# Kernel optimization log

Measured on AMD Instinct MI355X. Metric: run time of the kernel, lower is better.

The kernel has to match this reference:

```python
import jax, jax.numpy as jnp
import numpy as np

SIZE = 84        # pupil size
SIZE_F = 167     # field grid size
X_PAD = 39       # pad for 90 -> 167
KNUM = 16        # number of phase kernels (== required batch size)
CENTER = 120     # center crop
NOISE = 0.003


def _disk_mask(M=SIZE, R=SIZE / 2.0):
    # get_amp: unit disk of radius R on an MxM grid
    x, y = np.meshgrid(np.arange(-(M - 1) / 2, M / 2), np.arange(-(M - 1) / 2, M / 2))
    return jnp.asarray((x ** 2 + y ** 2 <= R ** 2).astype(np.float32))


def setup_inputs() -> dict:
    key = jax.random.key(0)
    k1, k2, k3 = jax.random.split(key, 3)
    x = jax.random.uniform(k1, (16, 90, 90, 1), dtype=jnp.float32)
    P = jax.random.uniform(k2, (16, 84, 84), dtype=jnp.float32,
                           minval=-0.5 * np.pi, maxval=0.5 * np.pi)
    W3 = jax.random.normal(k3, (12800, 10), dtype=jnp.float32) * 0.01
    b3 = jnp.zeros((10,), dtype=jnp.float32)
    return {"x": x, "P": P, "W3": W3, "b3": b3}


def _forward(x, P, W3, b3):
    mask = _disk_mask()
    amp = jnp.sum(mask)  # normalization of the autocorrelation

    # --- input field: pad 90 -> 167, complex, fftshift/fft2/fftshift ---
    # NOTE: tf.signal.fftshift default shifts ALL axes (incl. batch); the two
    # shifts cancel on the batch axis, replicated faithfully here.
    xp = jnp.pad(x, ((0, 0), (X_PAD, X_PAD - 1), (X_PAD, X_PAD - 1), (0, 0)))[..., 0]
    xc = xp.astype(jnp.complex64)
    X = jnp.fft.fftshift(jnp.fft.fft2(jnp.fft.fftshift(xc)))  # [16,167,167]
    Xr = jnp.repeat(X, KNUM, axis=0)                          # [256,167,167]

    # --- OTF: FFT-accelerated autocorrelation of the pupil P_amp*exp(i*phase) ---
    Pc = (mask * jnp.cos(P) + 1j * mask * jnp.sin(P)).astype(jnp.complex64)  # [16,84,84]
    Pp = jnp.pad(Pc, ((0, 0), (42, 41), (42, 41)))                           # [16,167,167]
    F = jnp.fft.fft2(Pp)
    OTF = jnp.fft.fftshift(jnp.fft.ifft2(F * jnp.conj(F)))  # all-axes shift
    OTF = jnp.concatenate([OTF[8:], OTF[:8]], axis=0) / amp  # undoes batch roll

    # --- propagation: multiply in frequency domain, back to space ---
    y = Xr * jnp.tile(OTF, (KNUM, 1, 1))  # [256,167,167]
    y = jnp.fft.fftshift(jnp.fft.ifft2(jnp.fft.fftshift(y)))
    r = jnp.real(y).reshape(16, KNUM, SIZE_F, SIZE_F)
    # per image: kernels 0..7 minus kernels 8..15 -> channels
    d = jnp.transpose(r[:, :8] - r[:, 8:], (0, 2, 3, 1))  # [16,167,167,8]

    # additive noise (np.random in original; fixed key -> deterministic constant)
    d = d + NOISE * jax.random.normal(jax.random.key(42), d.shape, dtype=jnp.float32)

    # center crop, relu, 3x3/3 max-pool, flatten, softmax dense
    b = (SIZE_F + 1) // 2 - CENTER // 2  # 24
    c = jax.nn.relu(d[:, b:b + CENTER, b:b + CENTER, :])  # [16,120,120,8]
    pooled = jax.lax.reduce_window(c, -jnp.inf, jax.lax.max,
                                   (1, 3, 3, 1), (1, 3, 3, 1), 'VALID')  # [16,40,40,8]
    flat = pooled.reshape(16, -1)  # [16,12800]
    return jax.nn.softmax(flat @ W3 + b3)


def reference(x, P, W3, b3):
    return _forward(x, P, W3, b3)
```

## Files before the change

### kernel.cpp

```cpp
#include <hip/hip_runtime.h>
#include <math.h>

constexpr int N  = 167;
constexpr int NN = 167 * 167;
constexpr int NP = 90;
constexpr int MP = 84;
constexpr int CROP = 120;
constexpr int HCOL = 84;
constexpr int HALF_SZ = 1784896;

constexpr size_t SZ_MAT   = (size_t)NN * 2;
constexpr size_t OFF_M1   = 0;
constexpr size_t OFF_M1T  = OFF_M1 + SZ_MAT;
constexpr size_t OFF_WF   = OFF_M1T + SZ_MAT;
constexpr size_t OFF_M2   = OFF_WF + SZ_MAT;
constexpr size_t OFF_M2T  = OFF_M2 + SZ_MAT;
constexpr size_t OFF_M3   = OFF_M2T + SZ_MAT;
constexpr size_t OFF_M3T84= OFF_M3 + (size_t)CROP * N * 2;
constexpr size_t OFF_PHI2 = OFF_M3T84 + (size_t)HCOL * CROP * 2;
constexpr size_t OFF_AMP  = OFF_PHI2 + (size_t)N * 2;
constexpr size_t OFF_X    = OFF_AMP + 2;
constexpr size_t OFF_T1   = OFF_X  + (size_t)16 * N * HCOL * 2;
constexpr size_t OFF_A    = OFF_T1 + (size_t)16 * N * NP * 2;
constexpr size_t OFF_T2   = OFF_A  + (size_t)16 * NN * 2;
constexpr size_t OFF_BD   = OFF_T2 + (size_t)16 * N * MP * 2;
constexpr size_t OFF_T3   = OFF_BD + (size_t)8 * NN;
constexpr size_t OFF_OTF  = OFF_T3 + (size_t)8 * N * HCOL * 2;
constexpr size_t OFF_FLAT = OFF_OTF+ (size_t)8 * N * HCOL * 2;
constexpr size_t OFF_PC   = OFF_FLAT + (size_t)16 * 12800;
constexpr size_t WS_FLOATS = OFF_PC + (size_t)16 * MP * MP * 2;

__device__ __forceinline__ unsigned rotl32(unsigned x, int r) {
    return (x << r) | (x >> (32 - r));
}

__device__ float noise_at(unsigned idx) {
    unsigned c0, c1; int lane;
    if (idx < (unsigned)HALF_SZ) { c0 = idx; c1 = idx + HALF_SZ; lane = 0; }
    else                         { c0 = idx - HALF_SZ; c1 = idx; lane = 1; }
    const unsigned ks0 = 0u, ks1 = 42u, ks2 = 0x1BD11BDAu ^ 42u;
    unsigned x0 = c0 + ks0, x1 = c1 + ks1;
#define TFR(r) { x0 += x1; x1 = rotl32(x1, r); x1 ^= x0; }
    TFR(13) TFR(15) TFR(26) TFR(6)   x0 += ks1; x1 += ks2 + 1u;
    TFR(17) TFR(29) TFR(16) TFR(24)  x0 += ks2; x1 += ks0 + 2u;
    TFR(13) TFR(15) TFR(26) TFR(6)   x0 += ks0; x1 += ks1 + 3u;
    TFR(17) TFR(29) TFR(16) TFR(24)  x0 += ks1; x1 += ks2 + 4u;
    TFR(13) TFR(15) TFR(26) TFR(6)   x0 += ks2; x1 += ks0 + 5u;
#undef TFR
    unsigned bits = lane ? x1 : x0;
    float u01 = __uint_as_float((bits >> 9) | 0x3F800000u) - 1.0f;
    const float lo = -0.99999994f;
    float f = fmaxf(lo, u01 * 2.0f + lo);
    float w = -log1pf(-f * f);
    float p;
    if (w < 5.0f) {
        w -= 2.5f;
        p = 2.81022636e-08f;
        p = fmaf(p, w, 3.43273939e-07f);
        p = fmaf(p, w, -3.5233877e-06f);
        p = fmaf(p, w, -4.39150654e-06f);
        p = fmaf(p, w, 0.00021858087f);
        p = fmaf(p, w, -0.00125372503f);
        p = fmaf(p, w, -0.00417768164f);
        p = fmaf(p, w, 0.246640727f);
        p = fmaf(p, w, 1.50140941f);
    } else {
        w = sqrtf(w) - 3.0f;
        p = -0.000200214257f;
        p = fmaf(p, w, 0.000100950558f);
        p = fmaf(p, w, 0.00134934322f);
        p = fmaf(p, w, -0.00367342844f);
        p = fmaf(p, w, 0.00573950773f);
        p = fmaf(p, w, -0.0076224613f);
        p = fmaf(p, w, 0.00943887047f);
        p = fmaf(p, w, 1.00167406f);
        p = fmaf(p, w, 2.83297682f);
    }
    return 1.41421356237f * p * f;
}

__global__ void k_prep(const float* __restrict__ P, float* ws) {
    int bx = blockIdx.x, t = threadIdx.x;
    if (bx < 109) {
        int id = bx * 256 + t;
        if (id >= NN) return;
        int k = id / N, m = id % N;
        const float TPI = (float)(6.283185307179586476925286766559 / 167.0);
        float s1, c1, sw, cw, s2, c2;
        int t1 = (int)(((long long)(k + 84) * ((m + 83) % N)) % N);
        sincosf(TPI * (float)t1, &s1, &c1);
        ws[OFF_M1 + 2 * id] = c1;  ws[OFF_M1 + 2 * id + 1] = -s1;
        ws[OFF_M1T + 2 * (m * N + k)] = c1;  ws[OFF_M1T + 2 * (m * N + k) + 1] = -s1;
        int tw = (int)(((long long)k * m) % N);
        sincosf(TPI * (float)tw, &sw, &cw);
        ws[OFF_WF + 2 * id] = cw;  ws[OFF_WF + 2 * id + 1] = -sw;
        int t2 = (int)(((long long)(k + 84) * m) % N);
        sincosf(TPI * (float)t2, &s2, &c2);
        const float inv = 1.0f / 167.0f;
        ws[OFF_M2 + 2 * id] = c2 * inv;  ws[OFF_M2 + 2 * id + 1] = s2 * inv;
        ws[OFF_M2T + 2 * (m * N + k)] = c2 * inv;  ws[OFF_M2T + 2 * (m * N + k) + 1] = s2 * inv;
        if (k < CROP) {
            int t3 = (int)(((long long)(k + 108) * ((m + 83) % N)) % N);
            float s3, c3;
            sincosf(TPI * (float)t3, &s3, &c3);
            ws[OFF_M3 + 2 * (k * N + m)] = c3 * inv;  ws[OFF_M3 + 2 * (k * N + m) + 1] = s3 * inv;
            if (m < HCOL) {
                ws[OFF_M3T84 + 2 * (m * CROP + k)] = c3 * inv;
                ws[OFF_M3T84 + 2 * (m * CROP + k) + 1] = s3 * inv;
            }
        }
        if (id < N) {
            int tp = (2 * id) % N;
            float sp, cp;
            sincosf(TPI * (float)tp, &sp, &cp);
            ws[OFF_PHI2 + 2 * id] = cp;
            ws[OFF_PHI2 + 2 * id + 1] = sp;
        }
    } else if (bx < 550) {
        int id = (bx - 109) * 256 + t;
        if (id >= 16 * MP * MP) return;
        int rc = id % (MP * MP);
        int r = rc / MP, c = rc % MP;
        float y = r - 41.5f, x = c - 41.5f;
        float2 v = {0.f, 0.f};
        if (x * x + y * y <= 1764.0f) {
            float sp, cp; sincosf(P[id], &sp, &cp);
            v.x = cp; v.y = sp;
        }
        ((float2*)(ws + OFF_PC))[id] = v;
    } else {
        __shared__ int red[256];
        int cnt = 0;
        for (int i = t; i < MP * MP; i += 256) {
            int r = i / MP, c = i % MP;
            float y = r - 41.5f, x = c - 41.5f;
            if (x * x + y * y <= 1764.0f) cnt++;
        }
        red[t] = cnt; __syncthreads();
        for (int s = 128; s > 0; s >>= 1) { if (t < s) red[t] += red[t + s]; __syncthreads(); }
        if (t == 0) ws[OFF_AMP] = (float)red[0];
    }
}

__global__ __launch_bounds__(128) void k_rows(const float* __restrict__ x, float* ws) {
    int kr = blockIdx.x, bj = blockIdx.y, t = threadIdx.x;
    __shared__ float2 wbuf[NP];
    if (blockIdx.z == 0) {
        const float2* M1 = (const float2*)(ws + OFF_M1);
        if (t < NP) wbuf[t] = M1[kr * N + 39 + t];
        __syncthreads();
        if (t >= NP) return;
        float2 acc = {0.f, 0.f};
        for (int nr = 0; nr < NP; nr++) {
            float2 w = wbuf[nr];
            float xv = x[(bj * NP + nr) * NP + t];
            acc.x += w.x * xv; acc.y += w.y * xv;
        }
        ((float2*)(ws + OFF_T1))[(bj * N + kr) * NP + t] = acc;
    } else {
        const float2* WF = (const float2*)(ws + OFF_WF);
        if (t < MP) wbuf[t] = WF[kr * N + 42 + t];
        __syncthreads();
        if (t >= MP) return;
        const float2* PC = (const float2*)(ws + OFF_PC) + (size_t)bj * MP * MP;
        float2 acc = {0.f, 0.f};
        for (int nr = 0; nr < MP; nr++) {
            float2 w = wbuf[nr];
            float2 pc = PC[nr * MP + t];
            acc.x += w.x * pc.x - w.y * pc.y;
            acc.y += w.x * pc.y + w.y * pc.x;
        }
        ((float2*)(ws + OFF_T2))[(bj * N + kr) * MP + t] = acc;
    }
}

constexpr int RCH = 6;
__global__ __launch_bounds__(192) void k_cols(float* ws) {
    int bj = blockIdx.y, tid = threadIdx.x;
    __shared__ float2 sbuf[RCH * MP];
    if (blockIdx.x < 84) {
        int k0 = blockIdx.x * 2;
        const float2* T1 = (const float2*)(ws + OFF_T1);
        for (int idx = tid; idx < 2 * NP; idx += 192) {
            int r = idx / NP, m = idx % NP;
            if (k0 + r < N) sbuf[r * NP + m] = T1[((size_t)bj * N + k0 + r) * NP + m];
        }
        __syncthreads();
        int col = tid % HCOL, grp = tid / HCOL;
        if (grp >= 2) return;
        int kr = k0 + grp;
        if (kr >= N) return;
        const float2* M1T = (const float2*)(ws + OFF_M1T);
        float2 acc = {0.f, 0.f};
        for (int nc = 0; nc < NP; nc++) {
            float2 u = sbuf[grp * NP + nc];
            float2 w = M1T[(39 + nc) * N + col];
            acc.x += u.x * w.x - u.y * w.y;
            acc.y += u.x * w.y + u.y * w.x;
        }
        ((float2*)(ws + OFF_X))[((size_t)bj * N + kr) * HCOL + col] = acc;
    } else {
        int i0 = (blockIdx.x - 84) * RCH;
        const float2* T2 = (const float2*)(ws + OFF_T2);
        for (int idx = tid; idx < RCH * MP; idx += 192) {
            int q = idx / MP, nc = idx % MP, kr = i0 + q;
            if (kr < N) sbuf[idx] = T2[(bj * N + kr) * MP + nc];
        }
        __syncthreads();
        if (tid >= N) return;
        const float2* WF = (const float2*)(ws + OFF_WF);
        float2 acc[RCH];
#pragma unroll
        for (int q = 0; q < RCH; q++) acc[q] = make_float2(0.f, 0.f);
        for (int nc = 0; nc < MP; nc++) {
            float2 w = WF[(42 + nc) * N + tid];
#pragma unroll
            for (int q = 0; q < RCH; q++) {
                float2 u = sbuf[q * MP + nc];
                acc[q].x += u.x * w.x - u.y * w.y;
                acc[q].y += u.x * w.y + u.y * w.x;
            }
        }
        float2* A = (float2*)(ws + OFF_A);
#pragma unroll
        for (int q = 0; q < RCH; q++)
            if (i0 + q < N) A[((size_t)bj * N + i0 + q) * N + tid] = acc[q];
    }
}

__global__ __launch_bounds__(192) void k2c(float* ws) {
    int chunk = blockIdx.x, c = blockIdx.y, tid = threadIdx.x;
    int k0 = chunk * 2;
    __shared__ float bds[2][N];
    const float2* A = (const float2*)(ws + OFF_A);
    float inv_amp = 1.0f / ws[OFF_AMP];
    for (int idx = tid; idx < 2 * N; idx += 192) {
        int r = idx / N, m = idx % N;
        int k = k0 + r;
        if (k < N) {
            float2 a0 = A[((size_t)c * N + k) * N + m];
            float2 a1 = A[((size_t)(c + 8) * N + k) * N + m];
            bds[r][m] = (a0.x * a0.x + a0.y * a0.y - a1.x * a1.x - a1.y * a1.y) * inv_amp;
        }
    }
    __syncthreads();
    int col = tid % HCOL, grp = tid / HCOL;
    if (grp >= 2) return;
    int k = k0 + grp;
    if (k >= N) return;
    const float2* M2T = (const float2*)(ws + OFF_M2T);
    float2 acc = {0.f, 0.f};
    for (int m = 0; m < N; m++) {
        float bv = bds[grp][m];
        float2 w = M2T[m * N + col];
        acc.x += w.x * bv; acc.y += w.y * bv;
    }
    ((float2*)(ws + OFF_T3))[((size_t)c * N + k) * HCOL + col] = acc;
}

__global__ __launch_bounds__(192) void k2d(float* ws) {
    int chunk = blockIdx.x, c = blockIdx.y, tid = threadIdx.x;
    int i0 = chunk * 2;
    __shared__ float2 m2s[2][N];
    const float2* M2 = (const float2*)(ws + OFF_M2);
    for (int idx = tid; idx < 2 * N; idx += 192) {
        int r = idx / N, k = idx % N;
        if (i0 + r < N) m2s[r][k] = M2[(i0 + r) * N + k];
    }
    __syncthreads();
    int col = tid % HCOL, grp = tid / HCOL;
    if (grp >= 2) return;
    int i = i0 + grp;
    if (i >= N) return;
    const float2* T3 = (const float2*)(ws + OFF_T3) + (size_t)c * N * HCOL;
    float2 acc = {0.f, 0.f};
    for (int k = 0; k < N; k++) {
        float2 w = m2s[grp][k];
        float2 u = T3[k * HCOL + col];
        acc.x += u.x * w.x - u.y * w.y;
        acc.y += u.x * w.y + u.y * w.x;
    }
    ((float2*)(ws + OFF_OTF))[((size_t)c * N + i) * HCOL + col] = acc;
}

constexpr int K34R = 12;
constexpr int KCH  = 16;
__global__ __launch_bounds__(256) void k34(float* ws) {
    int chunk = blockIdx.x, c = blockIdx.y, b = blockIdx.z, tid = threadIdx.x;
    int i0 = chunk * K34R;
    __shared__ __align__(16) float2 zs[KCH][HCOL];
    __shared__ float2 m3c[K34R][KCH];
    __shared__ __align__(16) float2 us[K34R][HCOL];
    __shared__ float2 phis[N];
    __shared__ float pm[4][CROP];
    const float2* M3  = (const float2*)(ws + OFF_M3);
    const float2* X   = (const float2*)(ws + OFF_X)   + (size_t)b * N * HCOL;
    const float2* OTF = (const float2*)(ws + OFF_OTF) + (size_t)c * N * HCOL;
    for (int idx = tid; idx < N; idx += 256) phis[idx] = ((const float2*)(ws + OFF_PHI2))[idx];

    int p = tid % 42, grp = tid / 42;
    int r0 = grp * 2, r1 = r0 + 1;
    float2 a00 = {0.f,0.f}, a01 = {0.f,0.f}, a10 = {0.f,0.f}, a11 = {0.f,0.f};

    for (int kr0 = 0; kr0 < N; kr0 += KCH) {
        int chn = min(KCH, N - kr0);
        __syncthreads();
        for (int idx = tid; idx < chn * HCOL; idx += 256) {
            int kl = idx / HCOL, col = idx % HCOL;
            float2 xv = X[(kr0 + kl) * HCOL + col];
            float2 ov = OTF[(kr0 + kl) * HCOL + col];
            zs[kl][col] = make_float2(xv.x * ov.x - xv.y * ov.y,
                                      xv.x * ov.y + xv.y * ov.x);
        }
        for (int idx = tid; idx < K34R * KCH; idx += 256) {
            int r = idx / KCH, kl = idx % KCH;
            if (kl < chn) m3c[r][kl] = M3[(i0 + r) * N + kr0 + kl];
        }
        __syncthreads();
        if (grp < 6) {
#pragma unroll 4
            for (int kl = 0; kl < chn; kl++) {
                float4 zz = *(const float4*)&zs[kl][2 * p];
                float2 w0 = m3c[r0][kl], w1 = m3c[r1][kl];
                a00.x += w0.x * zz.x - w0.y * zz.y;  a00.y += w0.x * zz.y + w0.y * zz.x;
                a01.x += w0.x * zz.z - w0.y * zz.w;  a01.y += w0.x * zz.w + w0.y * zz.z;
                a10.x += w1.x * zz.x - w1.y * zz.y;  a10.y += w1.x * zz.y + w1.y * zz.x;
                a11.x += w1.x * zz.z - w1.y * zz.w;  a11.y += w1.x * zz.w + w1.y * zz.z;
            }
        }
    }
    __syncthreads();
    if (grp < 6) {
        us[r0][2 * p] = a00;  us[r0][2 * p + 1] = a01;
        us[r1][2 * p] = a10;  us[r1][2 * p + 1] = a11;
    }
    __syncthreads();
    if (tid < 240) {
        int grp2 = tid / CROP, j = tid % CROP;
        int rbase = grp2 * 6;
        const float2* M3T84 = (const float2*)(ws + OFF_M3T84);
        float2 A[6]; float Bq[6];
#pragma unroll
        for (int q = 0; q < 6; q++) A[q] = make_float2(0.f, 0.f);
        for (int nc = 0; nc < HCOL - 1; nc++) {
            float2 w = M3T84[nc * CROP + j];
#pragma unroll
            for (int q = 0; q < 6; q++) {
                float2 u = us[rbase + q][nc];
                A[q].x += u.x * w.x - u.y * w.y;
                A[q].y += u.x * w.y + u.y * w.x;
            }
        }
        {
            float2 w = M3T84[(HCOL - 1) * CROP + j];
#pragma unroll
            for (int q = 0; q < 6; q++) {
                float2 u = us[rbase + q][HCOL - 1];
                Bq[q] = u.x * w.x - u.y * w.y;
            }
        }
#pragma unroll
        for (int g = 0; g < 2; g++) {
            float vmax = 0.f;
#pragma unroll
            for (int r = 0; r < 3; r++) {
                int q = g * 3 + r, i = i0 + rbase + q;
                int s = i + j + 49; if (s >= N) s -= N;
                float2 ph = phis[s];
                float val = A[q].x * (1.0f + ph.x) - A[q].y * ph.y + Bq[q];
                unsigned idx = (((unsigned)b * N + (24 + i)) * N + (24 + j)) * 8u + c;
                val += 0.003f * noise_at(idx);
                vmax = fmaxf(vmax, val);
            }
            pm[grp2 * 2 + g][j] = vmax;
        }
    }
    __syncthreads();
    if (tid < 160) {
        int pr = tid / 40, pc = tid % 40;
        float m = fmaxf(fmaxf(pm[pr][3 * pc], pm[pr][3 * pc + 1]), pm[pr][3 * pc + 2]);
        int prow = chunk * 4 + pr;
        ws[OFF_FLAT + (size_t)b * 12800 + ((size_t)prow * 40 + pc) * 8 + c] = m;
    }
}

__global__ void k5(const float* __restrict__ W3, const float* __restrict__ b3,
                   const float* __restrict__ ws, float* __restrict__ out) {
    int b = blockIdx.x, t = threadIdx.x;
    __shared__ float red[256][10];
    float acc[10];
#pragma unroll
    for (int o = 0; o < 10; o++) acc[o] = 0.f;
    const float* fl = ws + OFF_FLAT + (size_t)b * 12800;
    for (int f = t; f < 12800; f += 256) {
        float v = fl[f];
#pragma unroll
        for (int o = 0; o < 10; o++) acc[o] = fmaf(v, W3[f * 10 + o], acc[o]);
    }
#pragma unroll
    for (int o = 0; o < 10; o++) red[t][o] = acc[o];
    __syncthreads();
    for (int s = 128; s > 0; s >>= 1) {
        if (t < s) {
#pragma unroll
            for (int o = 0; o < 10; o++) red[t][o] += red[t + s][o];
        }
        __syncthreads();
    }
    if (t == 0) {
        float lg[10], mx = -1e30f;
#pragma unroll
        for (int o = 0; o < 10; o++) { lg[o] = red[0][o] + b3[o]; mx = fmaxf(mx, lg[o]); }
        float sum = 0.f;
#pragma unroll
        for (int o = 0; o < 10; o++) { lg[o] = expf(lg[o] - mx); sum += lg[o]; }
#pragma unroll
        for (int o = 0; o < 10; o++) out[b * 10 + o] = lg[o] / sum;
    }
}

extern "C" void kernel_launch(void* const* d_in, const int* in_sizes, int n_in,
                              void* d_out, int out_size, void* d_ws, size_t ws_size,
                              hipStream_t stream) {
    const float* x  = (const float*)d_in[0];
    const float* P  = (const float*)d_in[1];
    const float* W3 = (const float*)d_in[2];
    const float* b3 = (const float*)d_in[3];
    float* ws  = (float*)d_ws;
    float* out = (float*)d_out;

    k_prep<<<551, 256, 0, stream>>>(P, ws);
    k_rows<<<dim3(N, 16, 2), 128, 0, stream>>>(x, ws);
    k_cols<<<dim3(84 + 28, 16), 192, 0, stream>>>(ws);
    k2c<<<dim3(84, 8), 192, 0, stream>>>(ws);
    k2d<<<dim3(84, 8), 192, 0, stream>>>(ws);
    k34<<<dim3(CROP / K34R, 8, 16), 256, 0, stream>>>(ws);
    k5<<<16, 256, 0, stream>>>(W3, b3, ws, out);
}
```

Measured before the change: 210.7 us.

## Double-buffer k34 tiles, widen row block to 24, use twiddle table in prep

The main k34 kernel now processes 24 output rows per block instead of 12, with each thread computing a 4x2 register tile. The shared-memory tiles are double-buffered, so the next tile's global loads are issued into registers before computing on the current tile. This halves the number of blocks, which halves the redundant X*OTF product and phase reloads per row, and it hides load latency at the cost of more registers and shared memory. The prep kernel also replaces four sincosf calls per element with lookups into a 167-entry shared twiddle table.

```diff
diff --git a/kernel.cpp b/kernel.cpp
--- a/kernel.cpp
+++ b/kernel.cpp
@@ -82,39 +82,41 @@
 __global__ void k_prep(const float* __restrict__ P, float* ws) {
     int bx = blockIdx.x, t = threadIdx.x;
     if (bx < 109) {
+        __shared__ float2 wtab[N];
+        const float TPI = (float)(6.283185307179586476925286766559 / 167.0);
+        for (int i = t; i < N; i += 256) {
+            float s, c; sincosf(TPI * (float)i, &s, &c);
+            wtab[i] = make_float2(c, s);
+        }
+        __syncthreads();
         int id = bx * 256 + t;
         if (id >= NN) return;
         int k = id / N, m = id % N;
-        const float TPI = (float)(6.283185307179586476925286766559 / 167.0);
-        float s1, c1, sw, cw, s2, c2;
-        int t1 = (int)(((long long)(k + 84) * ((m + 83) % N)) % N);
-        sincosf(TPI * (float)t1, &s1, &c1);
-        ws[OFF_M1 + 2 * id] = c1;  ws[OFF_M1 + 2 * id + 1] = -s1;
-        ws[OFF_M1T + 2 * (m * N + k)] = c1;  ws[OFF_M1T + 2 * (m * N + k) + 1] = -s1;
-        int tw = (int)(((long long)k * m) % N);
-        sincosf(TPI * (float)tw, &sw, &cw);
-        ws[OFF_WF + 2 * id] = cw;  ws[OFF_WF + 2 * id + 1] = -sw;
-        int t2 = (int)(((long long)(k + 84) * m) % N);
-        sincosf(TPI * (float)t2, &s2, &c2);
         const float inv = 1.0f / 167.0f;
-        ws[OFF_M2 + 2 * id] = c2 * inv;  ws[OFF_M2 + 2 * id + 1] = s2 * inv;
-        ws[OFF_M2T + 2 * (m * N + k)] = c2 * inv;  ws[OFF_M2T + 2 * (m * N + k) + 1] = s2 * inv;
+        int t1 = ((k + 84) * ((m + 83) % N)) % N;
+        float2 w1 = wtab[t1];
+        ws[OFF_M1 + 2 * id] = w1.x;  ws[OFF_M1 + 2 * id + 1] = -w1.y;
+        ws[OFF_M1T + 2 * (m * N + k)] = w1.x;  ws[OFF_M1T + 2 * (m * N + k) + 1] = -w1.y;
+        int tw = (k * m) % N;
+        float2 ww = wtab[tw];
+        ws[OFF_WF + 2 * id] = ww.x;  ws[OFF_WF + 2 * id + 1] = -ww.y;
+        int t2 = ((k + 84) * m) % N;
+        float2 w2 = wtab[t2];
+        ws[OFF_M2 + 2 * id] = w2.x * inv;  ws[OFF_M2 + 2 * id + 1] = w2.y * inv;
+        ws[OFF_M2T + 2 * (m * N + k)] = w2.x * inv;  ws[OFF_M2T + 2 * (m * N + k) + 1] = w2.y * inv;
         if (k < CROP) {
-            int t3 = (int)(((long long)(k + 108) * ((m + 83) % N)) % N);
-            float s3, c3;
-            sincosf(TPI * (float)t3, &s3, &c3);
-            ws[OFF_M3 + 2 * (k * N + m)] = c3 * inv;  ws[OFF_M3 + 2 * (k * N + m) + 1] = s3 * inv;
+            int t3 = ((k + 108) * ((m + 83) % N)) % N;
+            float2 w3 = wtab[t3];
+            ws[OFF_M3 + 2 * (k * N + m)] = w3.x * inv;  ws[OFF_M3 + 2 * (k * N + m) + 1] = w3.y * inv;
             if (m < HCOL) {
-                ws[OFF_M3T84 + 2 * (m * CROP + k)] = c3 * inv;
-                ws[OFF_M3T84 + 2 * (m * CROP + k) + 1] = s3 * inv;
+                ws[OFF_M3T84 + 2 * (m * CROP + k)] = w3.x * inv;
+                ws[OFF_M3T84 + 2 * (m * CROP + k) + 1] = w3.y * inv;
             }
         }
         if (id < N) {
-            int tp = (2 * id) % N;
-            float sp, cp;
-            sincosf(TPI * (float)tp, &sp, &cp);
-            ws[OFF_PHI2 + 2 * id] = cp;
-            ws[OFF_PHI2 + 2 * id + 1] = sp;
+            float2 wp = wtab[(2 * id) % N];
+            ws[OFF_PHI2 + 2 * id] = wp.x;
+            ws[OFF_PHI2 + 2 * id + 1] = wp.y;
         }
     } else if (bx < 550) {
         int id = (bx - 109) * 256 + t;
@@ -283,69 +285,132 @@
     ((float2*)(ws + OFF_OTF))[((size_t)c * N + i) * HCOL + col] = acc;
 }
 
-constexpr int K34R = 12;
+constexpr int K34R = 24;
 constexpr int KCH  = 16;
+constexpr int NT34 = (N + KCH - 1) / KCH;
 __global__ __launch_bounds__(256) void k34(float* ws) {
     int chunk = blockIdx.x, c = blockIdx.y, b = blockIdx.z, tid = threadIdx.x;
     int i0 = chunk * K34R;
-    __shared__ __align__(16) float2 zs[KCH][HCOL];
-    __shared__ float2 m3c[K34R][KCH];
+    __shared__ __align__(16) float2 zs[2][KCH][HCOL];
+    __shared__ __align__(16) float2 m3c[2][KCH][K34R];
     __shared__ __align__(16) float2 us[K34R][HCOL];
     __shared__ float2 phis[N];
-    __shared__ float pm[4][CROP];
+    __shared__ float pm[8][CROP];
     const float2* M3  = (const float2*)(ws + OFF_M3);
     const float2* X   = (const float2*)(ws + OFF_X)   + (size_t)b * N * HCOL;
     const float2* OTF = (const float2*)(ws + OFF_OTF) + (size_t)c * N * HCOL;
     for (int idx = tid; idx < N; idx += 256) phis[idx] = ((const float2*)(ws + OFF_PHI2))[idx];
 
-    int p = tid % 42, grp = tid / 42;
-    int r0 = grp * 2, r1 = r0 + 1;
-    float2 a00 = {0.f,0.f}, a01 = {0.f,0.f}, a10 = {0.f,0.f}, a11 = {0.f,0.f};
-
-    for (int kr0 = 0; kr0 < N; kr0 += KCH) {
+    int pair = tid % 42, quad = tid / 42;
+    int r0 = quad * 4;
+    float2 acc[4][2];
+#pragma unroll
+    for (int j = 0; j < 4; j++) { acc[j][0] = make_float2(0.f, 0.f); acc[j][1] = make_float2(0.f, 0.f); }
+
+    float2 xr[6], og[6], m3r[2];
+
+    {
+        int cnt = KCH * HCOL;
+#pragma unroll
+        for (int e = 0; e < 6; e++) {
+            int idx = tid + e * 256;
+            if (idx < cnt) { int kl = idx / HCOL, col = idx % HCOL;
+                xr[e] = X[kl * HCOL + col]; og[e] = OTF[kl * HCOL + col]; }
+        }
+#pragma unroll
+        for (int e = 0; e < 2; e++) {
+            int idx = tid + e * 256;
+            if (idx < KCH * K34R) { int kl = idx & 15, r = idx >> 4;
+                m3r[e] = M3[(i0 + r) * N + kl]; }
+        }
+#pragma unroll
+        for (int e = 0; e < 6; e++) {
+            int idx = tid + e * 256;
+            if (idx < cnt) { int kl = idx / HCOL, col = idx % HCOL;
+                zs[0][kl][col] = make_float2(xr[e].x * og[e].x - xr[e].y * og[e].y,
+                                             xr[e].x * og[e].y + xr[e].y * og[e].x); }
+        }
+#pragma unroll
+        for (int e = 0; e < 2; e++) {
+            int idx = tid + e * 256;
+            if (idx < KCH * K34R) { int kl = idx & 15, r = idx >> 4; m3c[0][kl][r] = m3r[e]; }
+        }
+    }
+    __syncthreads();
+
+    for (int t = 0; t < NT34; t++) {
+        int cbuf = t & 1, nbuf = cbuf ^ 1;
+        int kr0 = t * KCH;
         int chn = min(KCH, N - kr0);
-        __syncthreads();
-        for (int idx = tid; idx < chn * HCOL; idx += 256) {
-            int kl = idx / HCOL, col = idx % HCOL;
-            float2 xv = X[(kr0 + kl) * HCOL + col];
-            float2 ov = OTF[(kr0 + kl) * HCOL + col];
-            zs[kl][col] = make_float2(xv.x * ov.x - xv.y * ov.y,
-                                      xv.x * ov.y + xv.y * ov.x);
-        }
-        for (int idx = tid; idx < K34R * KCH; idx += 256) {
-            int r = idx / KCH, kl = idx % KCH;
-            if (kl < chn) m3c[r][kl] = M3[(i0 + r) * N + kr0 + kl];
-        }
-        __syncthreads();
-        if (grp < 6) {
-#pragma unroll 4
+        int nbase = kr0 + KCH;
+        int ncnt = (t + 1 < NT34) ? (min(KCH, N - nbase) * HCOL) : 0;
+        if (t + 1 < NT34) {
+#pragma unroll
+            for (int e = 0; e < 6; e++) {
+                int idx = tid + e * 256;
+                if (idx < ncnt) { int kl = idx / HCOL, col = idx % HCOL;
+                    xr[e] = X[(nbase + kl) * HCOL + col]; og[e] = OTF[(nbase + kl) * HCOL + col]; }
+            }
+#pragma unroll
+            for (int e = 0; e < 2; e++) {
+                int idx = tid + e * 256;
+                if (idx < KCH * K34R) { int kl = idx & 15, r = idx >> 4;
+                    if (nbase + kl < N) m3r[e] = M3[(i0 + r) * N + nbase + kl]; }
+            }
+        }
+        if (quad < 6) {
             for (int kl = 0; kl < chn; kl++) {
-                float4 zz = *(const float4*)&zs[kl][2 * p];
-                float2 w0 = m3c[r0][kl], w1 = m3c[r1][kl];
-                a00.x += w0.x * zz.x - w0.y * zz.y;  a00.y += w0.x * zz.y + w0.y * zz.x;
-                a01.x += w0.x * zz.z - w0.y * zz.w;  a01.y += w0.x * zz.w + w0.y * zz.z;
-                a10.x += w1.x * zz.x - w1.y * zz.y;  a10.y += w1.x * zz.y + w1.y * zz.x;
-                a11.x += w1.x * zz.z - w1.y * zz.w;  a11.y += w1.x * zz.w + w1.y * zz.z;
-            }
+                float4 zz = *(const float4*)&zs[cbuf][kl][2 * pair];
+                float4 wa = *(const float4*)&m3c[cbuf][kl][r0];
+                float4 wb = *(const float4*)&m3c[cbuf][kl][r0 + 2];
+                acc[0][0].x += wa.x * zz.x - wa.y * zz.y;  acc[0][0].y += wa.x * zz.y + wa.y * zz.x;
+                acc[0][1].x += wa.x * zz.z - wa.y * zz.w;  acc[0][1].y += wa.x * zz.w + wa.y * zz.z;
+                acc[1][0].x += wa.z * zz.x - wa.w * zz.y;  acc[1][0].y += wa.z * zz.y + wa.w * zz.x;
+                acc[1][1].x += wa.z * zz.z - wa.w * zz.w;  acc[1][1].y += wa.z * zz.w + wa.w * zz.z;
+                acc[2][0].x += wb.x * zz.x - wb.y * zz.y;  acc[2][0].y += wb.x * zz.y + wb.y * zz.x;
+                acc[2][1].x += wb.x * zz.z - wb.y * zz.w;  acc[2][1].y += wb.x * zz.w + wb.y * zz.z;
+                acc[3][0].x += wb.z * zz.x - wb.w * zz.y;  acc[3][0].y += wb.z * zz.y + wb.w * zz.x;
+                acc[3][1].x += wb.z * zz.z - wb.w * zz.w;  acc[3][1].y += wb.z * zz.w + wb.w * zz.z;
+            }
+        }
+        if (t + 1 < NT34) {
+#pragma unroll
+            for (int e = 0; e < 6; e++) {
+                int idx = tid + e * 256;
+                if (idx < ncnt) { int kl = idx / HCOL, col = idx % HCOL;
+                    zs[nbuf][kl][col] = make_float2(xr[e].x * og[e].x - xr[e].y * og[e].y,
+                                                    xr[e].x * og[e].y + xr[e].y * og[e].x); }
+            }
+#pragma unroll
+            for (int e = 0; e < 2; e++) {
+                int idx = tid + e * 256;
+                if (idx < KCH * K34R) { int kl = idx & 15, r = idx >> 4;
+                    if (nbase + kl < N) m3c[nbuf][kl][r] = m3r[e]; }
+            }
+        }
+        __syncthreads();
+    }
+
+    if (quad < 6) {
+#pragma unroll
+        for (int j = 0; j < 4; j++) {
+            *(float4*)&us[r0 + j][2 * pair] =
+                make_float4(acc[j][0].x, acc[j][0].y, acc[j][1].x, acc[j][1].y);
         }
     }
     __syncthreads();
-    if (grp < 6) {
-        us[r0][2 * p] = a00;  us[r0][2 * p + 1] = a01;
-        us[r1][2 * p] = a10;  us[r1][2 * p + 1] = a11;
-    }
-    __syncthreads();
+
     if (tid < 240) {
         int grp2 = tid / CROP, j = tid % CROP;
-        int rbase = grp2 * 6;
+        int rbase = grp2 * 12;
         const float2* M3T84 = (const float2*)(ws + OFF_M3T84);
-        float2 A[6]; float Bq[6];
-#pragma unroll
-        for (int q = 0; q < 6; q++) A[q] = make_float2(0.f, 0.f);
+        float2 A[12]; float Bq[12];
+#pragma unroll
+        for (int q = 0; q < 12; q++) A[q] = make_float2(0.f, 0.f);
         for (int nc = 0; nc < HCOL - 1; nc++) {
             float2 w = M3T84[nc * CROP + j];
 #pragma unroll
-            for (int q = 0; q < 6; q++) {
+            for (int q = 0; q < 12; q++) {
                 float2 u = us[rbase + q][nc];
                 A[q].x += u.x * w.x - u.y * w.y;
                 A[q].y += u.x * w.y + u.y * w.x;
@@ -354,13 +419,13 @@
         {
             float2 w = M3T84[(HCOL - 1) * CROP + j];
 #pragma unroll
-            for (int q = 0; q < 6; q++) {
+            for (int q = 0; q < 12; q++) {
                 float2 u = us[rbase + q][HCOL - 1];
                 Bq[q] = u.x * w.x - u.y * w.y;
             }
         }
 #pragma unroll
-        for (int g = 0; g < 2; g++) {
+        for (int g = 0; g < 4; g++) {
             float vmax = 0.f;
 #pragma unroll
             for (int r = 0; r < 3; r++) {
@@ -372,14 +437,14 @@
                 val += 0.003f * noise_at(idx);
                 vmax = fmaxf(vmax, val);
             }
-            pm[grp2 * 2 + g][j] = vmax;
+            pm[grp2 * 4 + g][j] = vmax;
         }
     }
     __syncthreads();
-    if (tid < 160) {
-        int pr = tid / 40, pc = tid % 40;
+    for (int idx = tid; idx < 320; idx += 256) {
+        int pr = idx / 40, pc = idx % 40;
         float m = fmaxf(fmaxf(pm[pr][3 * pc], pm[pr][3 * pc + 1]), pm[pr][3 * pc + 2]);
-        int prow = chunk * 4 + pr;
+        int prow = chunk * 8 + pr;
         ws[OFF_FLAT + (size_t)b * 12800 + ((size_t)prow * 40 + pc) * 8 + c] = m;
     }
 }
```

Result: slower. 220.9 us (+4.9%).

## Prefetch next k34 tile into registers and tabulate twiddles in shared memory

Applied to the files above, without the earlier changes.

In k34, the next chunk of X, OTF and M3 is loaded into registers while the current shared tile is consumed, which overlaps global latency with compute. M3 tiles are transposed in shared memory so each thread reads both row weights with one float4 load. Separately, k_prep computes 167 sincos values once per block into a shared table and indexes it instead of calling sincosf for every matrix entry. The prefetch raises register pressure, and the table lookups change rounding slightly compared with direct sincos.

```diff
diff --git a/kernel.cpp b/kernel.cpp
--- a/kernel.cpp
+++ b/kernel.cpp
@@ -82,39 +82,41 @@
 __global__ void k_prep(const float* __restrict__ P, float* ws) {
     int bx = blockIdx.x, t = threadIdx.x;
     if (bx < 109) {
+        __shared__ float2 wtab[N];
+        const float TPI = (float)(6.283185307179586476925286766559 / 167.0);
+        for (int i = t; i < N; i += 256) {
+            float s, c; sincosf(TPI * (float)i, &s, &c);
+            wtab[i] = make_float2(c, s);
+        }
+        __syncthreads();
         int id = bx * 256 + t;
         if (id >= NN) return;
         int k = id / N, m = id % N;
-        const float TPI = (float)(6.283185307179586476925286766559 / 167.0);
-        float s1, c1, sw, cw, s2, c2;
-        int t1 = (int)(((long long)(k + 84) * ((m + 83) % N)) % N);
-        sincosf(TPI * (float)t1, &s1, &c1);
-        ws[OFF_M1 + 2 * id] = c1;  ws[OFF_M1 + 2 * id + 1] = -s1;
-        ws[OFF_M1T + 2 * (m * N + k)] = c1;  ws[OFF_M1T + 2 * (m * N + k) + 1] = -s1;
-        int tw = (int)(((long long)k * m) % N);
-        sincosf(TPI * (float)tw, &sw, &cw);
-        ws[OFF_WF + 2 * id] = cw;  ws[OFF_WF + 2 * id + 1] = -sw;
-        int t2 = (int)(((long long)(k + 84) * m) % N);
-        sincosf(TPI * (float)t2, &s2, &c2);
         const float inv = 1.0f / 167.0f;
-        ws[OFF_M2 + 2 * id] = c2 * inv;  ws[OFF_M2 + 2 * id + 1] = s2 * inv;
-        ws[OFF_M2T + 2 * (m * N + k)] = c2 * inv;  ws[OFF_M2T + 2 * (m * N + k) + 1] = s2 * inv;
+        int t1 = ((k + 84) * ((m + 83) % N)) % N;
+        float2 w1 = wtab[t1];
+        ws[OFF_M1 + 2 * id] = w1.x;  ws[OFF_M1 + 2 * id + 1] = -w1.y;
+        ws[OFF_M1T + 2 * (m * N + k)] = w1.x;  ws[OFF_M1T + 2 * (m * N + k) + 1] = -w1.y;
+        int tw = (k * m) % N;
+        float2 ww = wtab[tw];
+        ws[OFF_WF + 2 * id] = ww.x;  ws[OFF_WF + 2 * id + 1] = -ww.y;
+        int t2 = ((k + 84) * m) % N;
+        float2 w2 = wtab[t2];
+        ws[OFF_M2 + 2 * id] = w2.x * inv;  ws[OFF_M2 + 2 * id + 1] = w2.y * inv;
+        ws[OFF_M2T + 2 * (m * N + k)] = w2.x * inv;  ws[OFF_M2T + 2 * (m * N + k) + 1] = w2.y * inv;
         if (k < CROP) {
-            int t3 = (int)(((long long)(k + 108) * ((m + 83) % N)) % N);
-            float s3, c3;
-            sincosf(TPI * (float)t3, &s3, &c3);
-            ws[OFF_M3 + 2 * (k * N + m)] = c3 * inv;  ws[OFF_M3 + 2 * (k * N + m) + 1] = s3 * inv;
+            int t3 = ((k + 108) * ((m + 83) % N)) % N;
+            float2 w3 = wtab[t3];
+            ws[OFF_M3 + 2 * (k * N + m)] = w3.x * inv;  ws[OFF_M3 + 2 * (k * N + m) + 1] = w3.y * inv;
             if (m < HCOL) {
-                ws[OFF_M3T84 + 2 * (m * CROP + k)] = c3 * inv;
-                ws[OFF_M3T84 + 2 * (m * CROP + k) + 1] = s3 * inv;
+                ws[OFF_M3T84 + 2 * (m * CROP + k)] = w3.x * inv;
+                ws[OFF_M3T84 + 2 * (m * CROP + k) + 1] = w3.y * inv;
             }
         }
         if (id < N) {
-            int tp = (2 * id) % N;
-            float sp, cp;
-            sincosf(TPI * (float)tp, &sp, &cp);
-            ws[OFF_PHI2 + 2 * id] = cp;
-            ws[OFF_PHI2 + 2 * id + 1] = sp;
+            float2 wp = wtab[(2 * id) % N];
+            ws[OFF_PHI2 + 2 * id] = wp.x;
+            ws[OFF_PHI2 + 2 * id + 1] = wp.y;
         }
     } else if (bx < 550) {
         int id = (bx - 109) * 256 + t;
@@ -285,11 +287,12 @@
 
 constexpr int K34R = 12;
 constexpr int KCH  = 16;
+constexpr int NT34 = (N + KCH - 1) / KCH;
 __global__ __launch_bounds__(256) void k34(float* ws) {
     int chunk = blockIdx.x, c = blockIdx.y, b = blockIdx.z, tid = threadIdx.x;
     int i0 = chunk * K34R;
     __shared__ __align__(16) float2 zs[KCH][HCOL];
-    __shared__ float2 m3c[K34R][KCH];
+    __shared__ __align__(16) float2 m3c[KCH][K34R];
     __shared__ __align__(16) float2 us[K34R][HCOL];
     __shared__ float2 phis[N];
     __shared__ float pm[4][CROP];
@@ -298,43 +301,72 @@
     const float2* OTF = (const float2*)(ws + OFF_OTF) + (size_t)c * N * HCOL;
     for (int idx = tid; idx < N; idx += 256) phis[idx] = ((const float2*)(ws + OFF_PHI2))[idx];
 
-    int p = tid % 42, grp = tid / 42;
-    int r0 = grp * 2, r1 = r0 + 1;
+    int skl[6], scol[6];
+#pragma unroll
+    for (int e = 0; e < 6; e++) {
+        int idx = tid + e * 256;
+        skl[e] = idx / HCOL; scol[e] = idx - skl[e] * HCOL;
+    }
+    int mkl = tid & 15, mr = tid >> 4;
+
+    int pair = tid % 42, grp = tid / 42;
+    int r0 = grp * 2;
     float2 a00 = {0.f,0.f}, a01 = {0.f,0.f}, a10 = {0.f,0.f}, a11 = {0.f,0.f};
 
-    for (int kr0 = 0; kr0 < N; kr0 += KCH) {
+    float2 xr[6], og[6], m3r;
+
+#pragma unroll
+    for (int e = 0; e < 6; e++)
+        if (skl[e] < KCH) { xr[e] = X[skl[e] * HCOL + scol[e]]; og[e] = OTF[skl[e] * HCOL + scol[e]]; }
+    if (tid < 192) m3r = M3[(i0 + mr) * N + mkl];
+#pragma unroll
+    for (int e = 0; e < 6; e++)
+        if (skl[e] < KCH)
+            zs[skl[e]][scol[e]] = make_float2(xr[e].x * og[e].x - xr[e].y * og[e].y,
+                                              xr[e].x * og[e].y + xr[e].y * og[e].x);
+    if (tid < 192) m3c[mkl][mr] = m3r;
+    __syncthreads();
+
+    for (int t = 0; t < NT34; t++) {
+        int kr0 = t * KCH;
         int chn = min(KCH, N - kr0);
-        __syncthreads();
-        for (int idx = tid; idx < chn * HCOL; idx += 256) {
-            int kl = idx / HCOL, col = idx % HCOL;
-            float2 xv = X[(kr0 + kl) * HCOL + col];
-            float2 ov = OTF[(kr0 + kl) * HCOL + col];
-            zs[kl][col] = make_float2(xv.x * ov.x - xv.y * ov.y,
-                                      xv.x * ov.y + xv.y * ov.x);
-        }
-        for (int idx = tid; idx < K34R * KCH; idx += 256) {
-            int r = idx / KCH, kl = idx % KCH;
-            if (kl < chn) m3c[r][kl] = M3[(i0 + r) * N + kr0 + kl];
-        }
-        __syncthreads();
+        int nbase = kr0 + KCH;
+        int nchn = (t + 1 < NT34) ? (N - nbase < KCH ? N - nbase : KCH) : 0;
+        if (nchn > 0) {
+#pragma unroll
+            for (int e = 0; e < 6; e++)
+                if (skl[e] < nchn) { xr[e] = X[(nbase + skl[e]) * HCOL + scol[e]];
+                                     og[e] = OTF[(nbase + skl[e]) * HCOL + scol[e]]; }
+            if (tid < 192 && mkl < nchn) m3r = M3[(i0 + mr) * N + nbase + mkl];
+        }
         if (grp < 6) {
-#pragma unroll 4
             for (int kl = 0; kl < chn; kl++) {
-                float4 zz = *(const float4*)&zs[kl][2 * p];
-                float2 w0 = m3c[r0][kl], w1 = m3c[r1][kl];
-                a00.x += w0.x * zz.x - w0.y * zz.y;  a00.y += w0.x * zz.y + w0.y * zz.x;
-                a01.x += w0.x * zz.z - w0.y * zz.w;  a01.y += w0.x * zz.w + w0.y * zz.z;
-                a10.x += w1.x * zz.x - w1.y * zz.y;  a10.y += w1.x * zz.y + w1.y * zz.x;
-                a11.x += w1.x * zz.z - w1.y * zz.w;  a11.y += w1.x * zz.w + w1.y * zz.z;
-            }
-        }
-    }
-    __syncthreads();
+                float4 zz = *(const float4*)&zs[kl][2 * pair];
+                float4 wa = *(const float4*)&m3c[kl][r0];
+                a00.x += wa.x * zz.x - wa.y * zz.y;  a00.y += wa.x * zz.y + wa.y * zz.x;
+                a01.x += wa.x * zz.z - wa.y * zz.w;  a01.y += wa.x * zz.w + wa.y * zz.z;
+                a10.x += wa.z * zz.x - wa.w * zz.y;  a10.y += wa.z * zz.y + wa.w * zz.x;
+                a11.x += wa.z * zz.z - wa.w * zz.w;  a11.y += wa.z * zz.w + wa.w * zz.z;
+            }
+        }
+        __syncthreads();
+        if (nchn > 0) {
+#pragma unroll
+            for (int e = 0; e < 6; e++)
+                if (skl[e] < nchn)
+                    zs[skl[e]][scol[e]] = make_float2(xr[e].x * og[e].x - xr[e].y * og[e].y,
+                                                      xr[e].x * og[e].y + xr[e].y * og[e].x);
+            if (tid < 192 && mkl < nchn) m3c[mkl][mr] = m3r;
+            __syncthreads();
+        }
+    }
+
     if (grp < 6) {
-        us[r0][2 * p] = a00;  us[r0][2 * p + 1] = a01;
-        us[r1][2 * p] = a10;  us[r1][2 * p + 1] = a11;
-    }
-    __syncthreads();
+        *(float4*)&us[r0][2 * pair]     = make_float4(a00.x, a00.y, a01.x, a01.y);
+        *(float4*)&us[r0 + 1][2 * pair] = make_float4(a10.x, a10.y, a11.x, a11.y);
+    }
+    __syncthreads();
+
     if (tid < 240) {
         int grp2 = tid / CROP, j = tid % CROP;
         int rbase = grp2 * 6;
```

Result: no change. 211.1 us (+0.2%).
